# Kernel optimization log

Hardware: AMD Instinct MI355X
Metric: run time of the kernel (lower is better)

The kernel has to match this reference:

```python
import jax, jax.numpy as jnp
import numpy as np

N_WORDS, L_CHARS = 16384, 16
CHAR_SIZE, C_EMB = 128, 64
CONV_L, KERNEL, PAD = 256, 3, 2
VOCAB, D_EMB = 50000, 300
PAD_IDX = 1


def setup_inputs() -> dict:
    key = jax.random.key(0)
    k1, k2, k3, k4, k5, k6 = jax.random.split(key, 6)
    X = jax.random.randint(k1, (N_WORDS, L_CHARS), 0, CHAR_SIZE, dtype=jnp.int32)
    X_word = jax.random.randint(k2, (N_WORDS,), 0, VOCAB, dtype=jnp.int32)
    char_emb_w = jax.random.normal(k3, (CHAR_SIZE, C_EMB), dtype=jnp.float32)
    char_emb_w = char_emb_w.at[PAD_IDX].set(0.0)  # padding row zeroed, as in _init_char_embedding
    conv_w = jax.random.normal(k4, (CONV_L, C_EMB, KERNEL), dtype=jnp.float32) * 0.05
    conv_b = jax.random.normal(k5, (CONV_L,), dtype=jnp.float32) * 0.05
    word_emb_w = jax.random.normal(k6, (VOCAB, D_EMB), dtype=jnp.float32)
    return {"X": X, "X_word": X_word, "char_emb_w": char_emb_w,
            "conv_w": conv_w, "conv_b": conv_b, "word_emb_w": word_emb_w}


def reference(X, X_word, char_emb_w, conv_w, conv_b, word_emb_w):
    # char embedding lookup: [N, L, c_emb] -> NCH layout [N, c_emb, L]
    ce = char_emb_w[X].transpose(0, 2, 1)
    # Conv1d(c_emb -> conv_l, kernel=3, padding=2): out length L + 2*PAD - K + 1
    y = jax.lax.conv_general_dilated(
        ce, conv_w, window_strides=(1,), padding=[(PAD, PAD)],
        dimension_numbers=("NCH", "OIH", "NCH"))
    y = jax.nn.relu(y + conv_b[None, :, None])
    # MaxPool over the full time dimension -> [N, conv_l]
    char_feat = jnp.max(y, axis=2)
    # word embedding lookup: [N, d_emb]
    we = word_emb_w[X_word]
    return jnp.concatenate([char_feat, we], axis=1)
```

## Files before the change

kernel.cpp:

```cpp
#include <hip/hip_runtime.h>

#define N_WORDS   16384
#define L_CHARS   16
#define CHAR_SIZE 128
#define C_EMB     64
#define CONV_L    256
#define KERNEL_K  3
#define D_EMB     300
#define OUT_STRIDE (CONV_L + D_EMB)
#define CH_Q      64
#define SLICE_H   (CHAR_SIZE * KERNEL_K * CH_Q)

typedef _Float16 half8 __attribute__((ext_vector_type(8)));

static __device__ __forceinline__ half8 h8max(half8 a, half8 b) {
#if __has_builtin(__builtin_elementwise_max)
    return __builtin_elementwise_max(a, b);
#else
    half8 r;
    #pragma unroll
    for (int i = 0; i < 8; ++i) r[i] = a[i] > b[i] ? a[i] : b[i];
    return r;
#endif
}

__global__ void transpose_w(const float* __restrict__ w, float* __restrict__ Wt) {
    int tid = blockIdx.x * blockDim.x + threadIdx.x;
    if (tid >= CONV_L * C_EMB * KERNEL_K) return;
    int o = tid / (C_EMB * KERNEL_K);
    int r = tid - o * (C_EMB * KERNEL_K);
    int i = r / KERNEL_K;
    int k = r - i * KERNEL_K;
    Wt[i * (KERNEL_K * CONV_L) + k * CONV_L + o] = w[tid];
}

__global__ void build_table(const float* __restrict__ emb,
                            const float* __restrict__ Wt,
                            _Float16* __restrict__ Th) {
    int c = blockIdx.x / 3;
    int k = blockIdx.x % 3;
    int o = threadIdx.x;
    const float* erow = emb + c * C_EMB;
    float s = 0.f;
    #pragma unroll
    for (int i = 0; i < C_EMB; ++i)
        s += erow[i] * Wt[i * (KERNEL_K * CONV_L) + k * CONV_L + o];
    int q  = o >> 6;
    int oi = o & 63;
    Th[q * SLICE_H + c * (KERNEL_K * CH_Q) + k * CH_Q + oi] = (_Float16)s;
}

__global__ __launch_bounds__(256, 3)
void main_kernel(const int* __restrict__ X,
                 const int* __restrict__ Xw,
                 const _Float16* __restrict__ Th,
                 const float* __restrict__ conv_b,
                 const float* __restrict__ word_emb,
                 float* __restrict__ out,
                 int word_blocks) {
    __shared__ __align__(16) _Float16 Ts[SLICE_H];

    const int lane = threadIdx.x & 63;
    const int wv   = threadIdx.x >> 6;

    if ((int)blockIdx.x < word_blocks) {
        const int wavesTotal = word_blocks * 4;
        const int waveId = blockIdx.x * 4 + wv;
        for (int n = waveId; n < N_WORDS; n += wavesTotal) {
            int widx = Xw[n];
            const float4* src = (const float4*)(word_emb + (size_t)widx * D_EMB);
            float4* dst = (float4*)(out + (size_t)n * OUT_STRIDE + CONV_L);
            dst[lane] = src[lane];
            if (lane < (D_EMB / 4 - 64)) {
                dst[64 + lane] = src[64 + lane];
            }
        }
        return;
    }

    const int cb   = (int)blockIdx.x - word_blocks;
    const int q    = cb & 3;
    const int wgrp = cb >> 2;

    {
        const float4* src = (const float4*)(Th + q * SLICE_H);
        float4* dst = (float4*)Ts;
        #pragma unroll
        for (int i = 0; i < 12; ++i)
            dst[threadIdx.x + i * 256] = src[threadIdx.x + i * 256];
    }
    __syncthreads();

    const int g  = lane >> 3;
    const int l8 = lane & 7;

    float bias[8];
    {
        const float4* bp = (const float4*)(conv_b + q * CH_Q + l8 * 8);
        float4 b0 = bp[0], b1 = bp[1];
        bias[0]=b0.x; bias[1]=b0.y; bias[2]=b0.z; bias[3]=b0.w;
        bias[4]=b1.x; bias[5]=b1.y; bias[6]=b1.z; bias[7]=b1.w;
    }

    #pragma unroll
    for (int pass = 0; pass < 2; ++pass) {
        const int n = wgrp * 64 + pass * 32 + wv * 8 + g;

        const int4* xr = (const int4*)(X + n * L_CHARS);
        int4 q0 = xr[0], q1 = xr[1], q2 = xr[2], q3 = xr[3];
        int cs[16] = {q0.x, q0.y, q0.z, q0.w,
                      q1.x, q1.y, q1.z, q1.w,
                      q2.x, q2.y, q2.z, q2.w,
                      q3.x, q3.y, q3.z, q3.w};

        half8 a0 = (half8)(_Float16)0.f;
        half8 a1 = (half8)(_Float16)0.f;
        half8 m  = (half8)(_Float16)(-65504.f);

        #pragma unroll
        for (int j = 0; j < L_CHARS; ++j) {
            const _Float16* row = Ts + cs[j] * (KERNEL_K * CH_Q) + l8 * 8;
            half8 t0 = *(const half8*)(row);
            half8 t1 = *(const half8*)(row + CH_Q);
            half8 t2 = *(const half8*)(row + 2*CH_Q);
            half8 yj = a0 + t2;
            m  = h8max(m, yj);
            a0 = a1 + t1;
            a1 = t0;
        }
        m = h8max(m, a0);
        m = h8max(m, a1);

        float r[8];
        #pragma unroll
        for (int e = 0; e < 8; ++e)
            r[e] = fmaxf((float)m[e] + bias[e], 0.f);
        float4* dst = (float4*)(out + (size_t)n * OUT_STRIDE + q * CH_Q + l8 * 8);
        dst[0] = make_float4(r[0], r[1], r[2], r[3]);
        dst[1] = make_float4(r[4], r[5], r[6], r[7]);
    }
}

extern "C" void kernel_launch(void* const* d_in, const int* in_sizes, int n_in,
                              void* d_out, int out_size, void* d_ws, size_t ws_size,
                              hipStream_t stream) {
    const int*   X    = (const int*)d_in[0];
    const int*   Xw   = (const int*)d_in[1];
    const float* emb  = (const float*)d_in[2];
    const float* w    = (const float*)d_in[3];
    const float* b    = (const float*)d_in[4];
    const float* we   = (const float*)d_in[5];
    float* out = (float*)d_out;

    _Float16* Th = (_Float16*)d_ws;
    float*    Wt = (float*)((char*)d_ws + 4 * SLICE_H * sizeof(_Float16));

    transpose_w<<<(CONV_L * C_EMB * KERNEL_K + 255) / 256, 256, 0, stream>>>(w, Wt);
    build_table<<<CHAR_SIZE * KERNEL_K, 256, 0, stream>>>(emb, Wt, Th);

    const int WB = 256;
    const int CB = 1024;
    main_kernel<<<WB + CB, 256, 0, stream>>>(X, Xw, Th, b, we, out, WB);
}
```

Before: 132.7 us.

## Fuse table build kernels, double word-copy loads, prefetch char indices across four passes

The weight transpose and table-build kernels are merged into one kernel that stages the embeddings and one output channel's weights in shared memory, which removes a launch and the intermediate buffer. The word-embedding copy now issues loads for two words before storing, to keep more memory requests in flight. Char blocks are halved in number and each handles four passes of 32 words, with the next pass's character indices prefetched while the current one computes. This amortises the per-block table copy into LDS but gives fewer blocks for latency hiding.

```diff
diff --git a/kernel.cpp b/kernel.cpp
--- a/kernel.cpp
+++ b/kernel.cpp
@@ -24,30 +24,31 @@
 #endif
 }
 
-__global__ void transpose_w(const float* __restrict__ w, float* __restrict__ Wt) {
-    int tid = blockIdx.x * blockDim.x + threadIdx.x;
-    if (tid >= CONV_L * C_EMB * KERNEL_K) return;
-    int o = tid / (C_EMB * KERNEL_K);
-    int r = tid - o * (C_EMB * KERNEL_K);
-    int i = r / KERNEL_K;
-    int k = r - i * KERNEL_K;
-    Wt[i * (KERNEL_K * CONV_L) + k * CONV_L + o] = w[tid];
-}
+__global__ __launch_bounds__(384)
+void build_table_fused(const float* __restrict__ emb,
+                       const float* __restrict__ w,
+                       _Float16* __restrict__ Th) {
+    __shared__ float es[CHAR_SIZE * 65];
+    __shared__ float ws[C_EMB * KERNEL_K];
+    const int o = blockIdx.x;
 
-__global__ void build_table(const float* __restrict__ emb,
-                            const float* __restrict__ Wt,
-                            _Float16* __restrict__ Th) {
-    int c = blockIdx.x / 3;
-    int k = blockIdx.x % 3;
-    int o = threadIdx.x;
-    const float* erow = emb + c * C_EMB;
+    for (int idx = threadIdx.x; idx < CHAR_SIZE * C_EMB; idx += 384) {
+        int c = idx >> 6, i = idx & 63;
+        es[c * 65 + i] = emb[idx];
+    }
+    if (threadIdx.x < C_EMB * KERNEL_K)
+        ws[threadIdx.x] = w[o * (C_EMB * KERNEL_K) + threadIdx.x];
+    __syncthreads();
+
+    const int k = threadIdx.x >> 7;
+    const int c = threadIdx.x & 127;
     float s = 0.f;
     #pragma unroll
     for (int i = 0; i < C_EMB; ++i)
-        s += erow[i] * Wt[i * (KERNEL_K * CONV_L) + k * CONV_L + o];
-    int q  = o >> 6;
-    int oi = o & 63;
-    Th[q * SLICE_H + c * (KERNEL_K * CH_Q) + k * CH_Q + oi] = (_Float16)s;
+        s += es[c * 65 + i] * ws[i * KERNEL_K + k];
+
+    Th[(o >> 6) * SLICE_H + c * (KERNEL_K * CH_Q) + k * CH_Q + (o & 63)]
+        = (_Float16)s;
 }
 
 __global__ __launch_bounds__(256, 3)
@@ -66,14 +67,22 @@
     if ((int)blockIdx.x < word_blocks) {
         const int wavesTotal = word_blocks * 4;
         const int waveId = blockIdx.x * 4 + wv;
-        for (int n = waveId; n < N_WORDS; n += wavesTotal) {
-            int widx = Xw[n];
-            const float4* src = (const float4*)(word_emb + (size_t)widx * D_EMB);
-            float4* dst = (float4*)(out + (size_t)n * OUT_STRIDE + CONV_L);
-            dst[lane] = src[lane];
-            if (lane < (D_EMB / 4 - 64)) {
-                dst[64 + lane] = src[64 + lane];
-            }
+        for (int n = waveId; n < N_WORDS; n += 2 * wavesTotal) {
+            const int n2 = n + wavesTotal;
+            int w0 = Xw[n];
+            int w1 = Xw[n2];
+            const float4* s0 = (const float4*)(word_emb + (size_t)w0 * D_EMB);
+            const float4* s1 = (const float4*)(word_emb + (size_t)w1 * D_EMB);
+            const bool tail = lane < (D_EMB / 4 - 64);
+            float4 a0 = s0[lane], a1 = s1[lane];
+            float4 b0 = {}, b1 = {};
+            if (tail) { b0 = s0[64 + lane]; b1 = s1[64 + lane]; }
+            float4* d0 = (float4*)(out + (size_t)n  * OUT_STRIDE + CONV_L);
+            float4* d1 = (float4*)(out + (size_t)n2 * OUT_STRIDE + CONV_L);
+            d0[lane] = a0;
+            if (tail) d0[64 + lane] = b0;
+            d1[lane] = a1;
+            if (tail) d1[64 + lane] = b1;
         }
         return;
     }
@@ -102,16 +111,27 @@
         bias[4]=b1.x; bias[5]=b1.y; bias[6]=b1.z; bias[7]=b1.w;
     }
 
+    int4 c0, c1, c2, c3;
+    {
+        const int n0 = wgrp * 128 + wv * 8 + g;
+        const int4* xr = (const int4*)(X + n0 * L_CHARS);
+        c0 = xr[0]; c1 = xr[1]; c2 = xr[2]; c3 = xr[3];
+    }
+
     #pragma unroll
-    for (int pass = 0; pass < 2; ++pass) {
-        const int n = wgrp * 64 + pass * 32 + wv * 8 + g;
+    for (int pass = 0; pass < 4; ++pass) {
+        int4 p0 = c0, p1 = c1, p2 = c2, p3 = c3;
+        if (pass < 3) {
+            const int n1 = wgrp * 128 + (pass + 1) * 32 + wv * 8 + g;
+            const int4* xr = (const int4*)(X + n1 * L_CHARS);
+            p0 = xr[0]; p1 = xr[1]; p2 = xr[2]; p3 = xr[3];
+        }
 
-        const int4* xr = (const int4*)(X + n * L_CHARS);
-        int4 q0 = xr[0], q1 = xr[1], q2 = xr[2], q3 = xr[3];
-        int cs[16] = {q0.x, q0.y, q0.z, q0.w,
-                      q1.x, q1.y, q1.z, q1.w,
-                      q2.x, q2.y, q2.z, q2.w,
-                      q3.x, q3.y, q3.z, q3.w};
+        const int n = wgrp * 128 + pass * 32 + wv * 8 + g;
+        int cs[16] = {c0.x, c0.y, c0.z, c0.w,
+                      c1.x, c1.y, c1.z, c1.w,
+                      c2.x, c2.y, c2.z, c2.w,
+                      c3.x, c3.y, c3.z, c3.w};
 
         half8 a0 = (half8)(_Float16)0.f;
         half8 a1 = (half8)(_Float16)0.f;
@@ -138,6 +158,8 @@
         float4* dst = (float4*)(out + (size_t)n * OUT_STRIDE + q * CH_Q + l8 * 8);
         dst[0] = make_float4(r[0], r[1], r[2], r[3]);
         dst[1] = make_float4(r[4], r[5], r[6], r[7]);
+
+        c0 = p0; c1 = p1; c2 = p2; c3 = p3;
     }
 }
 
@@ -153,12 +175,10 @@
     float* out = (float*)d_out;
 
     _Float16* Th = (_Float16*)d_ws;
-    float*    Wt = (float*)((char*)d_ws + 4 * SLICE_H * sizeof(_Float16));
 
-    transpose_w<<<(CONV_L * C_EMB * KERNEL_K + 255) / 256, 256, 0, stream>>>(w, Wt);
-    build_table<<<CHAR_SIZE * KERNEL_K, 256, 0, stream>>>(emb, Wt, Th);
+    build_table_fused<<<CONV_L, 384, 0, stream>>>(emb, w, Th);
 
     const int WB = 256;
-    const int CB = 1024;
+    const int CB = 512;
     main_kernel<<<WB + CB, 256, 0, stream>>>(X, Xw, Th, b, we, out, WB);
 }
```

Result: faster. 123.5 us (-6.9%).
